# Kernel optimization log

Hardware: AMD Instinct MI355X
Metric: run time of the kernel (lower is better)

Reference implementation:

```python
import jax, jax.numpy as jnp
import numpy as np

B, S, M, D, H, L, FF = 2, 1024, 1024, 512, 8, 4, 2048
HD = D // H  # head dim 64
EPS = 1e-6   # fast_transformers linear-attention eps
LN_EPS = 1e-5


def setup_inputs() -> dict:
    key = jax.random.key(0)
    keys = iter(jax.random.split(key, 64))
    def w(shape, s=0.02):
        return jax.random.normal(next(keys), shape, dtype=jnp.float32) * s
    inp = {
        "memory": jax.random.normal(next(keys), (B, M, D), dtype=jnp.float32),
        "target": jax.random.normal(next(keys), (B, S, D), dtype=jnp.float32),
    }
    for p in ("sa", "ca"):
        for n in ("q", "k", "v", "o"):
            inp[f"{p}_W{n}"] = w((L, D, D))
            inp[f"{p}_b{n}"] = jnp.zeros((L, D), jnp.float32)
    inp["ff_W1"] = w((L, D, FF)); inp["ff_b1"] = jnp.zeros((L, FF), jnp.float32)
    inp["ff_W2"] = w((L, FF, D)); inp["ff_b2"] = jnp.zeros((L, D), jnp.float32)
    for n in ("ln1", "ln2", "ln3"):
        inp[f"{n}_g"] = jnp.ones((L, D), jnp.float32)
        inp[f"{n}_b"] = jnp.zeros((L, D), jnp.float32)
    inp["lnf_g"] = jnp.ones((D,), jnp.float32)
    inp["lnf_b"] = jnp.zeros((D,), jnp.float32)
    return inp


def _ln(x, g, b):
    m = x.mean(-1, keepdims=True)
    v = ((x - m) ** 2).mean(-1, keepdims=True)
    return (x - m) / jnp.sqrt(v + LN_EPS) * g + b


def _phi(x):  # elu feature map: elu(x) + 1
    return jax.nn.elu(x) + 1.0


def _heads(x, W, b):  # [b,s,D] -> [b,s,H,HD]
    y = x @ W + b
    return y.reshape(y.shape[0], y.shape[1], H, HD)


def _causal_linear_attn(q, k, v):
    # q,k already feature-mapped. cumulative KV state per step.
    kv = jnp.cumsum(jnp.einsum('bshd,bshm->bshdm', k, v), axis=1)  # [B,S,H,HD,HD]
    z = jnp.cumsum(k, axis=1)                                      # [B,S,H,HD]
    num = jnp.einsum('bshd,bshdm->bshm', q, kv)
    den = jnp.einsum('bshd,bshd->bsh', q, z) + EPS
    return num / den[..., None]


def _cross_linear_attn(q, k, v):
    kv = jnp.einsum('bmhd,bmhv->bhdv', k, v)  # [B,H,HD,HD]
    z = k.sum(axis=1)                          # [B,H,HD]
    num = jnp.einsum('bshd,bhdv->bshv', q, kv)
    den = jnp.einsum('bshd,bhd->bsh', q, z) + EPS
    return num / den[..., None]


def reference(memory, target,
              sa_Wq, sa_bq, sa_Wk, sa_bk, sa_Wv, sa_bv, sa_Wo, sa_bo,
              ca_Wq, ca_bq, ca_Wk, ca_bk, ca_Wv, ca_bv, ca_Wo, ca_bo,
              ff_W1, ff_b1, ff_W2, ff_b2,
              ln1_g, ln1_b, ln2_g, ln2_b, ln3_g, ln3_b, lnf_g, lnf_b):
    x = target
    for i in range(L):
        # causal linear self-attention
        q = _phi(_heads(x, sa_Wq[i], sa_bq[i]))
        k = _phi(_heads(x, sa_Wk[i], sa_bk[i]))
        v = _heads(x, sa_Wv[i], sa_bv[i])
        a = _causal_linear_attn(q, k, v).reshape(B, S, D) @ sa_Wo[i] + sa_bo[i]
        x = _ln(x + a, ln1_g[i], ln1_b[i])
        # linear cross-attention over memory
        q = _phi(_heads(x, ca_Wq[i], ca_bq[i]))
        k = _phi(_heads(memory, ca_Wk[i], ca_bk[i]))
        v = _heads(memory, ca_Wv[i], ca_bv[i])
        a = _cross_linear_attn(q, k, v).reshape(B, S, D) @ ca_Wo[i] + ca_bo[i]
        x = _ln(x + a, ln2_g[i], ln2_b[i])
        # gelu FFN
        y = jax.nn.gelu(x @ ff_W1[i] + ff_b1[i], approximate=False) @ ff_W2[i] + ff_b2[i]
        x = _ln(x + y, ln3_g[i], ln3_b[i])
    return _ln(x, lnf_g, lnf_b)
```

## Files before the change

### kernel.cpp

```cpp
#include <hip/hip_runtime.h>
#include <hip/hip_bf16.h>
#include <math.h>


typedef unsigned short u16;
typedef __bf16 bf16x8 __attribute__((ext_vector_type(8)));
typedef float f32x4v __attribute__((ext_vector_type(4)));

#define DEVI __device__ __forceinline__

DEVI float bf2f(u16 u) { return __uint_as_float(((unsigned)u) << 16); }
DEVI u16 f2bf(float f) {
  unsigned u = __float_as_uint(f);
  u += 0x7FFFu + ((u >> 16) & 1u);
  return (u16)(u >> 16);
}

__global__ __launch_bounds__(256) void transpose_f2b(
    const float* __restrict__ in, u16* __restrict__ out, int K, int N)
{
  __shared__ float tile[64 * 65];
  const size_t mat = (size_t)blockIdx.z * K * N;
  const int n0 = blockIdx.x * 64, k0 = blockIdx.y * 64;
  const int t = threadIdx.x;
#pragma unroll
  for (int p = 0; p < 16; ++p) {
    const int e = t + p * 256;
    const int lk = e >> 6, ln = e & 63;
    tile[lk * 65 + ln] = in[mat + (size_t)(k0 + lk) * N + n0 + ln];
  }
  __syncthreads();
#pragma unroll
  for (int p = 0; p < 16; ++p) {
    const int e = t + p * 256;
    const int ln = e >> 6, lk = e & 63;
    out[mat + (size_t)(n0 + ln) * K + k0 + lk] = f2bf(tile[lk * 65 + ln]);
  }
}

template<int ADT, int CDT>
__global__ __launch_bounds__(256) void gemm64(
    const void* __restrict__ A0, const void* __restrict__ A1, const void* __restrict__ A2,
    const u16* __restrict__ W0, const u16* __restrict__ W1, const u16* __restrict__ W2,
    const float* __restrict__ b0, const float* __restrict__ b1, const float* __restrict__ b2,
    void* __restrict__ C0, void* __restrict__ C1, void* __restrict__ C2,
    int acts, int N, int K, int lognyb)
{
  constexpr int LDT = 72;
  __shared__ __align__(16) u16 As[64 * LDT];
  __shared__ __align__(16) u16 Bs[64 * LDT];
  const int tid = threadIdx.x;
  const int by = blockIdx.y;
  const int seg = by >> lognyb;
  const int ny = by & ((1 << lognyb) - 1);
  const void* Av = seg == 0 ? A0 : (seg == 1 ? A1 : A2);
  const u16*  W  = seg == 0 ? W0 : (seg == 1 ? W1 : W2);
  const float* bias = seg == 0 ? b0 : (seg == 1 ? b1 : b2);
  void* Cv = seg == 0 ? C0 : (seg == 1 ? C1 : C2);
  const int act = (acts >> (2 * seg)) & 3;

  const int bm0 = blockIdx.x * 64, bn0 = ny * 64;
  const int lane = tid & 63, wid = tid >> 6;
  const int wr = wid >> 1, wc = wid & 1;
  const int l15 = lane & 15, lg = lane >> 4;
  const int srow = tid >> 2, scg = (tid & 3) * 16;
  f32x4v acc[2][2] = {};

  for (int k0 = 0; k0 < K; k0 += 64) {
    if (ADT == 0) {
      const float* A = (const float*)Av;
      const float* ap = &A[(size_t)(bm0 + srow) * K + k0 + scg];
#pragma unroll
      for (int i = 0; i < 4; ++i) {
        const float4 v = *(const float4*)&ap[i * 4];
        *(ushort4*)&As[srow * LDT + scg + i * 4] =
            make_ushort4(f2bf(v.x), f2bf(v.y), f2bf(v.z), f2bf(v.w));
      }
    } else {
      const u16* A = (const u16*)Av;
#pragma unroll
      for (int i = 0; i < 2; ++i)
        *(uint4*)&As[srow * LDT + scg + i * 8] =
            *(const uint4*)&A[(size_t)(bm0 + srow) * K + k0 + scg + i * 8];
    }
#pragma unroll
    for (int i = 0; i < 2; ++i)
      *(uint4*)&Bs[srow * LDT + scg + i * 8] =
          *(const uint4*)&W[(size_t)(bn0 + srow) * K + k0 + scg + i * 8];
    __syncthreads();
    bf16x8 af[2][2], bw[2][2];
#pragma unroll
    for (int kk = 0; kk < 2; ++kk) {
#pragma unroll
      for (int mm = 0; mm < 2; ++mm)
        af[kk][mm] = *(const bf16x8*)&As[(wr * 32 + mm * 16 + l15) * LDT + kk * 32 + lg * 8];
#pragma unroll
      for (int nn = 0; nn < 2; ++nn)
        bw[kk][nn] = *(const bf16x8*)&Bs[(wc * 32 + nn * 16 + l15) * LDT + kk * 32 + lg * 8];
    }
#pragma unroll
    for (int kk = 0; kk < 2; ++kk)
#pragma unroll
      for (int mm = 0; mm < 2; ++mm)
#pragma unroll
        for (int nn = 0; nn < 2; ++nn)
          acc[mm][nn] = __builtin_amdgcn_mfma_f32_16x16x32_bf16(af[kk][mm], bw[kk][nn], acc[mm][nn], 0, 0, 0);
    __syncthreads();
  }
#pragma unroll
  for (int nn = 0; nn < 2; ++nn) {
    const int col = bn0 + wc * 32 + nn * 16 + l15;
    const float bv = bias[col];
#pragma unroll
    for (int mm = 0; mm < 2; ++mm) {
#pragma unroll
      for (int r = 0; r < 4; ++r) {
        const int row = bm0 + wr * 32 + mm * 16 + lg * 4 + r;
        float v = acc[mm][nn][r] + bv;
        if (act == 1) v = v > 0.f ? v + 1.f : __expf(v);
        else if (act == 2) v = 0.5f * v * (1.f + erff(v * 0.70710678f));
        if (CDT == 0) ((float*)Cv)[(size_t)row * N + col] = v;
        else          ((u16*)Cv)[(size_t)row * N + col] = f2bf(v);
      }
    }
  }
}

__global__ __launch_bounds__(256) void lin_chunk_mfma(
    const float* __restrict__ kbuf, const float* __restrict__ vbuf,
    float* __restrict__ KVc, float* __restrict__ zc)
{
  constexpr int LDT = 72;
  __shared__ __align__(16) u16 Kt[64 * LDT];
  __shared__ __align__(16) u16 Vt[64 * LDT];
  const int c = blockIdx.x, bh = blockIdx.y;
  const int b = bh >> 3, h = bh & 7;
  const int t = threadIdx.x;
  const size_t rowbase = (size_t)(b * 1024 + c * 64);
  const int sp = t >> 4, colq = (t & 15) * 4;
#pragma unroll
  for (int pp = 0; pp < 2; ++pp) {
    const int s0 = pp * 32 + 2 * sp;
    const float4 ka = *(const float4*)&kbuf[(rowbase + s0) * 512 + h * 64 + colq];
    const float4 kb_ = *(const float4*)&kbuf[(rowbase + s0 + 1) * 512 + h * 64 + colq];
    const float4 va = *(const float4*)&vbuf[(rowbase + s0) * 512 + h * 64 + colq];
    const float4 vb_ = *(const float4*)&vbuf[(rowbase + s0 + 1) * 512 + h * 64 + colq];
    *(unsigned*)&Kt[(colq + 0) * LDT + s0] = (unsigned)f2bf(ka.x) | ((unsigned)f2bf(kb_.x) << 16);
    *(unsigned*)&Kt[(colq + 1) * LDT + s0] = (unsigned)f2bf(ka.y) | ((unsigned)f2bf(kb_.y) << 16);
    *(unsigned*)&Kt[(colq + 2) * LDT + s0] = (unsigned)f2bf(ka.z) | ((unsigned)f2bf(kb_.z) << 16);
    *(unsigned*)&Kt[(colq + 3) * LDT + s0] = (unsigned)f2bf(ka.w) | ((unsigned)f2bf(kb_.w) << 16);
    *(unsigned*)&Vt[(colq + 0) * LDT + s0] = (unsigned)f2bf(va.x) | ((unsigned)f2bf(vb_.x) << 16);
    *(unsigned*)&Vt[(colq + 1) * LDT + s0] = (unsigned)f2bf(va.y) | ((unsigned)f2bf(vb_.y) << 16);
    *(unsigned*)&Vt[(colq + 2) * LDT + s0] = (unsigned)f2bf(va.z) | ((unsigned)f2bf(vb_.z) << 16);
    *(unsigned*)&Vt[(colq + 3) * LDT + s0] = (unsigned)f2bf(va.w) | ((unsigned)f2bf(vb_.w) << 16);
  }
  __syncthreads();
  {
    const int zd = t >> 2, zg = t & 3;
    float zp = 0.f;
#pragma unroll
    for (int ss = 0; ss < 16; ++ss) zp += bf2f(Kt[zd * LDT + zg * 16 + ss]);
    zp += __shfl_xor(zp, 1, 64);
    zp += __shfl_xor(zp, 2, 64);
    if (zg == 0) zc[(size_t)(bh * 16 + c) * 64 + zd] = zp;
  }
  const int lane = t & 63, wid = t >> 6;
  const int wr = wid >> 1, wc = wid & 1;
  const int l15 = lane & 15, lg = lane >> 4;
  bf16x8 av[2][2], bk[2][2];
#pragma unroll
  for (int kk = 0; kk < 2; ++kk) {
#pragma unroll
    for (int mm = 0; mm < 2; ++mm)
      av[kk][mm] = *(const bf16x8*)&Vt[(wr * 32 + mm * 16 + l15) * LDT + kk * 32 + lg * 8];
#pragma unroll
    for (int nn = 0; nn < 2; ++nn)
      bk[kk][nn] = *(const bf16x8*)&Kt[(wc * 32 + nn * 16 + l15) * LDT + kk * 32 + lg * 8];
  }
  f32x4v acc[2][2] = {};
#pragma unroll
  for (int kk = 0; kk < 2; ++kk)
#pragma unroll
    for (int mm = 0; mm < 2; ++mm)
#pragma unroll
      for (int nn = 0; nn < 2; ++nn)
        acc[mm][nn] = __builtin_amdgcn_mfma_f32_16x16x32_bf16(av[kk][mm], bk[kk][nn], acc[mm][nn], 0, 0, 0);
  float* kvout = KVc + (size_t)(bh * 16 + c) * 4096;
#pragma unroll
  for (int mm = 0; mm < 2; ++mm)
#pragma unroll
    for (int r = 0; r < 4; ++r) {
      const int row = wr * 32 + mm * 16 + lg * 4 + r;
#pragma unroll
      for (int nn = 0; nn < 2; ++nn) {
        const int col = wc * 32 + nn * 16 + l15;
        kvout[row * 64 + col] = acc[mm][nn][r];
      }
    }
}

__global__ __launch_bounds__(256) void lin_scan_exclusive(
    float* __restrict__ KVc, float* __restrict__ zc,
    float* __restrict__ KVtot, float* __restrict__ ztot)
{
  const int grp = blockIdx.x, bh = blockIdx.y, t = threadIdx.x;
  const size_t base = (size_t)bh * 16 * 4096 + grp * 256 + t;
  float run = 0.f;
#pragma unroll
  for (int c = 0; c < 16; ++c) {
    const float tmp = KVc[base + (size_t)c * 4096];
    KVc[base + (size_t)c * 4096] = run;
    run += tmp;
  }
  KVtot[(size_t)bh * 4096 + grp * 256 + t] = run;
  if (grp == 0 && t < 64) {
    const size_t zb = (size_t)bh * 16 * 64 + t;
    float rz = 0.f;
#pragma unroll
    for (int c = 0; c < 16; ++c) {
      const float tmp = zc[zb + c * 64];
      zc[zb + c * 64] = rz;
      rz += tmp;
    }
    ztot[bh * 64 + t] = rz;
  }
}

__global__ __launch_bounds__(256) void sa_apply_mfma(
    const float* __restrict__ qbuf, const float* __restrict__ kbuf,
    const float* __restrict__ vbuf, const float* __restrict__ KVc,
    const float* __restrict__ zc, u16* __restrict__ out)
{
  constexpr int LDT = 72;
  __shared__ __align__(16) u16 Qs[64 * LDT];
  __shared__ __align__(16) u16 Ks[64 * LDT];
  __shared__ __align__(16) u16 Vt[64 * LDT];
  __shared__ __align__(16) u16 Ps[64 * LDT];
  __shared__ __align__(16) u16 KVs[64 * LDT];
  __shared__ float zp[64];
  __shared__ float den1[2][64];
  __shared__ float den2[64];
  const int c = blockIdx.x, bh = blockIdx.y;
  const int b = bh >> 3, h = bh & 7;
  const int t = threadIdx.x;
  const size_t rowbase = (size_t)(b * 1024 + c * 64);
  {
    const int srow = t >> 2, scg = (t & 3) * 16;
    const float* qp = &qbuf[(rowbase + srow) * 512 + h * 64 + scg];
    const float* kp = &kbuf[(rowbase + srow) * 512 + h * 64 + scg];
    const float* kvp = KVc + (size_t)(bh * 16 + c) * 4096 + srow * 64 + scg;
#pragma unroll
    for (int i = 0; i < 4; ++i) {
      const float4 a = *(const float4*)&qp[i * 4];
      *(ushort4*)&Qs[srow * LDT + scg + i * 4] = make_ushort4(f2bf(a.x), f2bf(a.y), f2bf(a.z), f2bf(a.w));
      const float4 bb = *(const float4*)&kp[i * 4];
      *(ushort4*)&Ks[srow * LDT + scg + i * 4] = make_ushort4(f2bf(bb.x), f2bf(bb.y), f2bf(bb.z), f2bf(bb.w));
      const float4 cc = *(const float4*)&kvp[i * 4];
      *(ushort4*)&KVs[srow * LDT + scg + i * 4] = make_ushort4(f2bf(cc.x), f2bf(cc.y), f2bf(cc.z), f2bf(cc.w));
    }
  }
  {
    const int sp = t >> 4, colq = (t & 15) * 4;
#pragma unroll
    for (int pp = 0; pp < 2; ++pp) {
      const int s0 = pp * 32 + 2 * sp;
      const float4 va = *(const float4*)&vbuf[(rowbase + s0) * 512 + h * 64 + colq];
      const float4 vb_ = *(const float4*)&vbuf[(rowbase + s0 + 1) * 512 + h * 64 + colq];
      *(unsigned*)&Vt[(colq + 0) * LDT + s0] = (unsigned)f2bf(va.x) | ((unsigned)f2bf(vb_.x) << 16);
      *(unsigned*)&Vt[(colq + 1) * LDT + s0] = (unsigned)f2bf(va.y) | ((unsigned)f2bf(vb_.y) << 16);
      *(unsigned*)&Vt[(colq + 2) * LDT + s0] = (unsigned)f2bf(va.z) | ((unsigned)f2bf(vb_.z) << 16);
      *(unsigned*)&Vt[(colq + 3) * LDT + s0] = (unsigned)f2bf(va.w) | ((unsigned)f2bf(vb_.w) << 16);
    }
  }
  if (t < 64) zp[t] = zc[(size_t)(bh * 16 + c) * 64 + t];
  __syncthreads();
  {
    const int di = t >> 2, dg = t & 3;
    float p2 = 0.f;
#pragma unroll
    for (int dd = 0; dd < 16; ++dd)
      p2 += bf2f(Qs[di * LDT + dg * 16 + dd]) * zp[dg * 16 + dd];
    p2 += __shfl_xor(p2, 1, 64);
    p2 += __shfl_xor(p2, 2, 64);
    if (dg == 0) den2[di] = p2;
  }
  const int lane = t & 63, wid = t >> 6;
  const int wr = wid >> 1, wc = wid & 1;
  const int l15 = lane & 15, lg = lane >> 4;
  bf16x8 af_q[2][2], bx[2][2];
#pragma unroll
  for (int kk = 0; kk < 2; ++kk) {
#pragma unroll
    for (int mm = 0; mm < 2; ++mm)
      af_q[kk][mm] = *(const bf16x8*)&Qs[(wr * 32 + mm * 16 + l15) * LDT + kk * 32 + lg * 8];
#pragma unroll
    for (int nn = 0; nn < 2; ++nn)
      bx[kk][nn] = *(const bf16x8*)&Ks[(wc * 32 + nn * 16 + l15) * LDT + kk * 32 + lg * 8];
  }
  f32x4v s_acc[2][2] = {};
#pragma unroll
  for (int kk = 0; kk < 2; ++kk)
#pragma unroll
    for (int mm = 0; mm < 2; ++mm)
#pragma unroll
      for (int nn = 0; nn < 2; ++nn)
        s_acc[mm][nn] = __builtin_amdgcn_mfma_f32_16x16x32_bf16(af_q[kk][mm], bx[kk][nn], s_acc[mm][nn], 0, 0, 0);
#pragma unroll
  for (int mm = 0; mm < 2; ++mm)
#pragma unroll
    for (int r = 0; r < 4; ++r) {
      const int row = wr * 32 + mm * 16 + lg * 4 + r;
      float dsum = 0.f;
#pragma unroll
      for (int nn = 0; nn < 2; ++nn) {
        const int col = wc * 32 + nn * 16 + l15;
        const float val = (col <= row) ? s_acc[mm][nn][r] : 0.f;
        Ps[row * LDT + col] = f2bf(val);
        dsum += val;
      }
      dsum += __shfl_xor(dsum, 1, 64);
      dsum += __shfl_xor(dsum, 2, 64);
      dsum += __shfl_xor(dsum, 4, 64);
      dsum += __shfl_xor(dsum, 8, 64);
      if (l15 == 0) den1[wc][row] = dsum;
    }
  __syncthreads();
  bf16x8 ap[2][2];
#pragma unroll
  for (int kk = 0; kk < 2; ++kk) {
#pragma unroll
    for (int mm = 0; mm < 2; ++mm)
      ap[kk][mm] = *(const bf16x8*)&Ps[(wr * 32 + mm * 16 + l15) * LDT + kk * 32 + lg * 8];
#pragma unroll
    for (int nn = 0; nn < 2; ++nn)
      bx[kk][nn] = *(const bf16x8*)&Vt[(wc * 32 + nn * 16 + l15) * LDT + kk * 32 + lg * 8];
  }
  f32x4v o_acc[2][2] = {};
#pragma unroll
  for (int kk = 0; kk < 2; ++kk)
#pragma unroll
    for (int mm = 0; mm < 2; ++mm)
#pragma unroll
      for (int nn = 0; nn < 2; ++nn)
        o_acc[mm][nn] = __builtin_amdgcn_mfma_f32_16x16x32_bf16(ap[kk][mm], bx[kk][nn], o_acc[mm][nn], 0, 0, 0);
#pragma unroll
  for (int kk = 0; kk < 2; ++kk)
#pragma unroll
    for (int nn = 0; nn < 2; ++nn)
      bx[kk][nn] = *(const bf16x8*)&KVs[(wc * 32 + nn * 16 + l15) * LDT + kk * 32 + lg * 8];
#pragma unroll
  for (int kk = 0; kk < 2; ++kk)
#pragma unroll
    for (int mm = 0; mm < 2; ++mm)
#pragma unroll
      for (int nn = 0; nn < 2; ++nn)
        o_acc[mm][nn] = __builtin_amdgcn_mfma_f32_16x16x32_bf16(af_q[kk][mm], bx[kk][nn], o_acc[mm][nn], 0, 0, 0);
#pragma unroll
  for (int mm = 0; mm < 2; ++mm)
#pragma unroll
    for (int r = 0; r < 4; ++r) {
      const int row = wr * 32 + mm * 16 + lg * 4 + r;
      const float rden = 1.f / (den1[0][row] + den1[1][row] + den2[row] + 1e-6f);
#pragma unroll
      for (int nn = 0; nn < 2; ++nn) {
        const int col = wc * 32 + nn * 16 + l15;
        out[(rowbase + row) * 512 + h * 64 + col] = f2bf(o_acc[mm][nn][r] * rden);
      }
    }
}

__global__ __launch_bounds__(256) void ca_apply_mfma(
    const float* __restrict__ qbuf, const float* __restrict__ KVtot,
    const float* __restrict__ ztot, u16* __restrict__ out)
{
  constexpr int LDT = 72;
  __shared__ __align__(16) u16 Qs[64 * LDT];
  __shared__ __align__(16) u16 KVs[64 * LDT];
  __shared__ float zt[64];
  __shared__ float den2[64];
  const int c = blockIdx.x, bh = blockIdx.y;
  const int b = bh >> 3, h = bh & 7;
  const int t = threadIdx.x;
  const size_t rowbase = (size_t)(b * 1024 + c * 64);
  {
    const int srow = t >> 2, scg = (t & 3) * 16;
    const float* qp = &qbuf[(rowbase + srow) * 512 + h * 64 + scg];
    const float* kvp = KVtot + (size_t)bh * 4096 + srow * 64 + scg;
#pragma unroll
    for (int i = 0; i < 4; ++i) {
      const float4 a = *(const float4*)&qp[i * 4];
      *(ushort4*)&Qs[srow * LDT + scg + i * 4] = make_ushort4(f2bf(a.x), f2bf(a.y), f2bf(a.z), f2bf(a.w));
      const float4 cc = *(const float4*)&kvp[i * 4];
      *(ushort4*)&KVs[srow * LDT + scg + i * 4] = make_ushort4(f2bf(cc.x), f2bf(cc.y), f2bf(cc.z), f2bf(cc.w));
    }
  }
  if (t < 64) zt[t] = ztot[bh * 64 + t];
  __syncthreads();
  {
    const int di = t >> 2, dg = t & 3;
    float p2 = 0.f;
#pragma unroll
    for (int dd = 0; dd < 16; ++dd)
      p2 += bf2f(Qs[di * LDT + dg * 16 + dd]) * zt[dg * 16 + dd];
    p2 += __shfl_xor(p2, 1, 64);
    p2 += __shfl_xor(p2, 2, 64);
    if (dg == 0) den2[di] = p2;
  }
  const int lane = t & 63, wid = t >> 6;
  const int wr = wid >> 1, wc = wid & 1;
  const int l15 = lane & 15, lg = lane >> 4;
  bf16x8 aq[2][2], bkv[2][2];
#pragma unroll
  for (int kk = 0; kk < 2; ++kk) {
#pragma unroll
    for (int mm = 0; mm < 2; ++mm)
      aq[kk][mm] = *(const bf16x8*)&Qs[(wr * 32 + mm * 16 + l15) * LDT + kk * 32 + lg * 8];
#pragma unroll
    for (int nn = 0; nn < 2; ++nn)
      bkv[kk][nn] = *(const bf16x8*)&KVs[(wc * 32 + nn * 16 + l15) * LDT + kk * 32 + lg * 8];
  }
  f32x4v o_acc[2][2] = {};
#pragma unroll
  for (int kk = 0; kk < 2; ++kk)
#pragma unroll
    for (int mm = 0; mm < 2; ++mm)
#pragma unroll
      for (int nn = 0; nn < 2; ++nn)
        o_acc[mm][nn] = __builtin_amdgcn_mfma_f32_16x16x32_bf16(aq[kk][mm], bkv[kk][nn], o_acc[mm][nn], 0, 0, 0);
  __syncthreads();
#pragma unroll
  for (int mm = 0; mm < 2; ++mm)
#pragma unroll
    for (int r = 0; r < 4; ++r) {
      const int row = wr * 32 + mm * 16 + lg * 4 + r;
      const float rden = 1.f / (den2[row] + 1e-6f);
#pragma unroll
      for (int nn = 0; nn < 2; ++nn) {
        const int col = wc * 32 + nn * 16 + l15;
        out[(rowbase + row) * 512 + h * 64 + col] = f2bf(o_acc[mm][nn][r] * rden);
      }
    }
}

__global__ __launch_bounds__(256) void ln_residual(
    float* __restrict__ x, const float* __restrict__ a,
    const float* __restrict__ g, const float* __restrict__ bt)
{
  const int t = threadIdx.x, lane = t & 63, w = t >> 6;
  const int row = blockIdx.x * 4 + w;
  float* xr = x + (size_t)row * 512;
  const float* ar = a + (size_t)row * 512;
  float4 x0 = *(const float4*)&xr[lane * 8];
  float4 x1 = *(const float4*)&xr[lane * 8 + 4];
  float4 a0 = *(const float4*)&ar[lane * 8];
  float4 a1 = *(const float4*)&ar[lane * 8 + 4];
  float v[8];
  v[0] = x0.x + a0.x; v[1] = x0.y + a0.y; v[2] = x0.z + a0.z; v[3] = x0.w + a0.w;
  v[4] = x1.x + a1.x; v[5] = x1.y + a1.y; v[6] = x1.z + a1.z; v[7] = x1.w + a1.w;
  float s = 0.f, sq = 0.f;
#pragma unroll
  for (int i = 0; i < 8; ++i) { s += v[i]; sq += v[i] * v[i]; }
#pragma unroll
  for (int off = 32; off > 0; off >>= 1) {
    s += __shfl_xor(s, off, 64);
    sq += __shfl_xor(sq, off, 64);
  }
  const float mean = s * (1.f / 512.f);
  const float var = sq * (1.f / 512.f) - mean * mean;
  const float rstd = rsqrtf(var + 1e-5f);
  float o[8];
#pragma unroll
  for (int i = 0; i < 8; ++i) {
    const int col = lane * 8 + i;
    o[i] = (v[i] - mean) * rstd * g[col] + bt[col];
  }
  *(float4*)&xr[lane * 8]     = make_float4(o[0], o[1], o[2], o[3]);
  *(float4*)&xr[lane * 8 + 4] = make_float4(o[4], o[5], o[6], o[7]);
}

__global__ __launch_bounds__(256) void ln_final(
    const float* __restrict__ x, const float* __restrict__ g,
    const float* __restrict__ bt, float* __restrict__ out)
{
  const int t = threadIdx.x, lane = t & 63, w = t >> 6;
  const int row = blockIdx.x * 4 + w;
  const float* xr = x + (size_t)row * 512;
  float4 x0 = *(const float4*)&xr[lane * 8];
  float4 x1 = *(const float4*)&xr[lane * 8 + 4];
  float v[8] = { x0.x, x0.y, x0.z, x0.w, x1.x, x1.y, x1.z, x1.w };
  float s = 0.f, sq = 0.f;
#pragma unroll
  for (int i = 0; i < 8; ++i) { s += v[i]; sq += v[i] * v[i]; }
#pragma unroll
  for (int off = 32; off > 0; off >>= 1) {
    s += __shfl_xor(s, off, 64);
    sq += __shfl_xor(sq, off, 64);
  }
  const float mean = s * (1.f / 512.f);
  const float var = sq * (1.f / 512.f) - mean * mean;
  const float rstd = rsqrtf(var + 1e-5f);
  float o[8];
#pragma unroll
  for (int i = 0; i < 8; ++i) {
    const int col = lane * 8 + i;
    o[i] = (v[i] - mean) * rstd * g[col] + bt[col];
  }
  *(float4*)&out[(size_t)row * 512 + lane * 8]     = make_float4(o[0], o[1], o[2], o[3]);
  *(float4*)&out[(size_t)row * 512 + lane * 8 + 4] = make_float4(o[4], o[5], o[6], o[7]);
}

extern "C" void kernel_launch(void* const* d_in, const int* in_sizes, int n_in,
                              void* d_out, int out_size, void* d_ws, size_t ws_size,
                              hipStream_t stream)
{
  (void)in_sizes; (void)n_in; (void)out_size; (void)ws_size;
  constexpr int Dm = 512, Lc = 4, FFc = 2048;

  const float* memory = (const float*)d_in[0];
  const float* target = (const float*)d_in[1];
  const float *saW[4], *sab[4], *caW[4], *cab[4];
  for (int j = 0; j < 4; ++j) {
    saW[j] = (const float*)d_in[2 + 2 * j];
    sab[j] = (const float*)d_in[3 + 2 * j];
    caW[j] = (const float*)d_in[10 + 2 * j];
    cab[j] = (const float*)d_in[11 + 2 * j];
  }
  const float* ffW1 = (const float*)d_in[18];
  const float* ffb1 = (const float*)d_in[19];
  const float* ffW2 = (const float*)d_in[20];
  const float* ffb2 = (const float*)d_in[21];
  const float* lng[4] = { (const float*)d_in[22], (const float*)d_in[24],
                          (const float*)d_in[26], (const float*)d_in[28] };
  const float* lnb[4] = { (const float*)d_in[23], (const float*)d_in[25],
                          (const float*)d_in[27], (const float*)d_in[29] };

  size_t off = 0;
  auto alloc = [&](size_t bytes) -> void* {
    void* p = (char*)d_ws + off;
    off += (bytes + 255) & ~(size_t)255;
    return p;
  };
  u16* WtS[4]; u16* WtC[4];
  for (int j = 0; j < 4; ++j) WtS[j] = (u16*)alloc((size_t)Lc * Dm * Dm * 2);
  for (int j = 0; j < 4; ++j) WtC[j] = (u16*)alloc((size_t)Lc * Dm * Dm * 2);
  u16* WtF1 = (u16*)alloc((size_t)Lc * Dm * FFc * 2);
  u16* WtF2 = (u16*)alloc((size_t)Lc * FFc * Dm * 2);
  float* x    = (float*)alloc((size_t)2048 * 512 * 4);
  float* qb   = (float*)alloc((size_t)2048 * 512 * 4);
  float* kb   = (float*)alloc((size_t)2048 * 512 * 4);
  float* vb   = (float*)alloc((size_t)2048 * 512 * 4);
  u16*   attn = (u16*)alloc((size_t)2048 * 512 * 2);
  u16*   ffh  = (u16*)alloc((size_t)2048 * 2048 * 2);
  float* KVc  = (float*)alloc((size_t)16 * 16 * 4096 * 4);
  float* zcb  = (float*)alloc((size_t)16 * 16 * 64 * 4);
  float* KVtot= (float*)alloc((size_t)16 * 4096 * 4);
  float* ztot = (float*)alloc((size_t)16 * 64 * 4);

  for (int j = 0; j < 4; ++j) {
    transpose_f2b<<<dim3(8, 8, 4), 256, 0, stream>>>(saW[j], WtS[j], Dm, Dm);
    transpose_f2b<<<dim3(8, 8, 4), 256, 0, stream>>>(caW[j], WtC[j], Dm, Dm);
  }
  transpose_f2b<<<dim3(32, 8, 4), 256, 0, stream>>>(ffW1, WtF1, Dm, FFc);
  transpose_f2b<<<dim3(8, 32, 4), 256, 0, stream>>>(ffW2, WtF2, FFc, Dm);

  hipMemcpyAsync(x, target, (size_t)2048 * 512 * 4, hipMemcpyDeviceToDevice, stream);

  for (int i = 0; i < Lc; ++i) {
    const size_t wo  = (size_t)i * Dm * Dm;
    const size_t wo1 = (size_t)i * Dm * FFc;
    const size_t wo2 = (size_t)i * FFc * Dm;
    gemm64<0, 0><<<dim3(32, 24), 256, 0, stream>>>(
        x, x, x, WtS[0] + wo, WtS[1] + wo, WtS[2] + wo,
        sab[0] + i * Dm, sab[1] + i * Dm, sab[2] + i * Dm,
        qb, kb, vb, 0x05, 512, 512, 3);
    lin_chunk_mfma<<<dim3(16, 16), 256, 0, stream>>>(kb, vb, KVc, zcb);
    lin_scan_exclusive<<<dim3(16, 16), 256, 0, stream>>>(KVc, zcb, KVtot, ztot);
    sa_apply_mfma<<<dim3(16, 16), 256, 0, stream>>>(qb, kb, vb, KVc, zcb, attn);
    gemm64<1, 0><<<dim3(32, 8), 256, 0, stream>>>(
        attn, attn, attn, WtS[3] + wo, WtS[3] + wo, WtS[3] + wo,
        sab[3] + i * Dm, sab[3] + i * Dm, sab[3] + i * Dm,
        qb, qb, qb, 0, 512, 512, 3);
    ln_residual<<<512, 256, 0, stream>>>(x, qb, lng[0] + i * Dm, lnb[0] + i * Dm);
    gemm64<0, 0><<<dim3(32, 24), 256, 0, stream>>>(
        x, memory, memory, WtC[0] + wo, WtC[1] + wo, WtC[2] + wo,
        cab[0] + i * Dm, cab[1] + i * Dm, cab[2] + i * Dm,
        qb, kb, vb, 0x05, 512, 512, 3);
    lin_chunk_mfma<<<dim3(16, 16), 256, 0, stream>>>(kb, vb, KVc, zcb);
    lin_scan_exclusive<<<dim3(16, 16), 256, 0, stream>>>(KVc, zcb, KVtot, ztot);
    ca_apply_mfma<<<dim3(16, 16), 256, 0, stream>>>(qb, KVtot, ztot, attn);
    gemm64<1, 0><<<dim3(32, 8), 256, 0, stream>>>(
        attn, attn, attn, WtC[3] + wo, WtC[3] + wo, WtC[3] + wo,
        cab[3] + i * Dm, cab[3] + i * Dm, cab[3] + i * Dm,
        qb, qb, qb, 0, 512, 512, 3);
    ln_residual<<<512, 256, 0, stream>>>(x, qb, lng[1] + i * Dm, lnb[1] + i * Dm);
    gemm64<0, 1><<<dim3(32, 32), 256, 0, stream>>>(
        x, x, x, WtF1 + wo1, WtF1 + wo1, WtF1 + wo1,
        ffb1 + i * FFc, ffb1 + i * FFc, ffb1 + i * FFc,
        ffh, ffh, ffh, 2, 2048, 512, 5);
    gemm64<1, 0><<<dim3(32, 8), 256, 0, stream>>>(
        ffh, ffh, ffh, WtF2 + wo2, WtF2 + wo2, WtF2 + wo2,
        ffb2 + i * Dm, ffb2 + i * Dm, ffb2 + i * Dm,
        qb, qb, qb, 0, 512, 2048, 3);
    ln_residual<<<512, 256, 0, stream>>>(x, qb, lng[2] + i * Dm, lnb[2] + i * Dm);
  }
  ln_final<<<512, 256, 0, stream>>>(x, lng[3], lnb[3], (float*)d_out);
}
```

Baseline: 682.1 us.

## Keep activations in bf16 between kernels and double-buffer GEMM shared tiles

LayerNorm now also writes a bf16 copy of the hidden state, memory and target are cast once up front, and Q/K/V projections are stored as bf16. GEMMs and attention kernels then read bf16 directly instead of loading fp32 and converting. The GEMM also gains a register-prefetched, double-buffered LDS pipeline with one barrier per K step and a launch-bounds occupancy hint. This halves intermediate traffic and removes conversion work, but rounds q/k/v before the attention kernels and uses more shared memory per block.

Result: faster. 605.6 us (-11.2%).

```diff
diff --git a/kernel.cpp b/kernel.cpp
--- a/kernel.cpp
+++ b/kernel.cpp
@@ -38,23 +38,37 @@
   }
 }
 
-template<int ADT, int CDT>
-__global__ __launch_bounds__(256) void gemm64(
-    const void* __restrict__ A0, const void* __restrict__ A1, const void* __restrict__ A2,
+__global__ __launch_bounds__(256) void cast_dual(
+    const float* __restrict__ in, float* __restrict__ fout, u16* __restrict__ bout)
+{
+  const int i = blockIdx.x * 256 + threadIdx.x;
+  const float4 a = ((const float4*)in)[i * 2];
+  const float4 b = ((const float4*)in)[i * 2 + 1];
+  if (fout) {
+    ((float4*)fout)[i * 2] = a;
+    ((float4*)fout)[i * 2 + 1] = b;
+  }
+  ((ushort4*)bout)[i * 2]     = make_ushort4(f2bf(a.x), f2bf(a.y), f2bf(a.z), f2bf(a.w));
+  ((ushort4*)bout)[i * 2 + 1] = make_ushort4(f2bf(b.x), f2bf(b.y), f2bf(b.z), f2bf(b.w));
+}
+
+template<int CDT>
+__global__ __launch_bounds__(256, 4) void gemm64(
+    const u16* __restrict__ A0, const u16* __restrict__ A1, const u16* __restrict__ A2,
     const u16* __restrict__ W0, const u16* __restrict__ W1, const u16* __restrict__ W2,
     const float* __restrict__ b0, const float* __restrict__ b1, const float* __restrict__ b2,
     void* __restrict__ C0, void* __restrict__ C1, void* __restrict__ C2,
     int acts, int N, int K, int lognyb)
 {
   constexpr int LDT = 72;
-  __shared__ __align__(16) u16 As[64 * LDT];
-  __shared__ __align__(16) u16 Bs[64 * LDT];
+  __shared__ __align__(16) u16 As[2][64 * LDT];
+  __shared__ __align__(16) u16 Bs[2][64 * LDT];
   const int tid = threadIdx.x;
   const int by = blockIdx.y;
   const int seg = by >> lognyb;
   const int ny = by & ((1 << lognyb) - 1);
-  const void* Av = seg == 0 ? A0 : (seg == 1 ? A1 : A2);
-  const u16*  W  = seg == 0 ? W0 : (seg == 1 ? W1 : W2);
+  const u16* A = seg == 0 ? A0 : (seg == 1 ? A1 : A2);
+  const u16* W = seg == 0 ? W0 : (seg == 1 ? W1 : W2);
   const float* bias = seg == 0 ? b0 : (seg == 1 ? b1 : b2);
   void* Cv = seg == 0 ? C0 : (seg == 1 ? C1 : C2);
   const int act = (acts >> (2 * seg)) & 3;
@@ -64,39 +78,38 @@
   const int wr = wid >> 1, wc = wid & 1;
   const int l15 = lane & 15, lg = lane >> 4;
   const int srow = tid >> 2, scg = (tid & 3) * 16;
+  const u16* Ap = A + (size_t)(bm0 + srow) * K + scg;
+  const u16* Wp = W + (size_t)(bn0 + srow) * K + scg;
+
+  uint4 ra0 = *(const uint4*)(Ap);
+  uint4 ra1 = *(const uint4*)(Ap + 8);
+  uint4 rb0 = *(const uint4*)(Wp);
+  uint4 rb1 = *(const uint4*)(Wp + 8);
+  *(uint4*)&As[0][srow * LDT + scg]     = ra0;
+  *(uint4*)&As[0][srow * LDT + scg + 8] = ra1;
+  *(uint4*)&Bs[0][srow * LDT + scg]     = rb0;
+  *(uint4*)&Bs[0][srow * LDT + scg + 8] = rb1;
+  __syncthreads();
+
   f32x4v acc[2][2] = {};
-
+  int cur = 0;
   for (int k0 = 0; k0 < K; k0 += 64) {
-    if (ADT == 0) {
-      const float* A = (const float*)Av;
-      const float* ap = &A[(size_t)(bm0 + srow) * K + k0 + scg];
-#pragma unroll
-      for (int i = 0; i < 4; ++i) {
-        const float4 v = *(const float4*)&ap[i * 4];
-        *(ushort4*)&As[srow * LDT + scg + i * 4] =
-            make_ushort4(f2bf(v.x), f2bf(v.y), f2bf(v.z), f2bf(v.w));
-      }
-    } else {
-      const u16* A = (const u16*)Av;
-#pragma unroll
-      for (int i = 0; i < 2; ++i)
-        *(uint4*)&As[srow * LDT + scg + i * 8] =
-            *(const uint4*)&A[(size_t)(bm0 + srow) * K + k0 + scg + i * 8];
-    }
-#pragma unroll
-    for (int i = 0; i < 2; ++i)
-      *(uint4*)&Bs[srow * LDT + scg + i * 8] =
-          *(const uint4*)&W[(size_t)(bn0 + srow) * K + k0 + scg + i * 8];
-    __syncthreads();
+    const bool more = (k0 + 64 < K);
+    if (more) {
+      ra0 = *(const uint4*)(Ap + k0 + 64);
+      ra1 = *(const uint4*)(Ap + k0 + 72);
+      rb0 = *(const uint4*)(Wp + k0 + 64);
+      rb1 = *(const uint4*)(Wp + k0 + 72);
+    }
     bf16x8 af[2][2], bw[2][2];
 #pragma unroll
     for (int kk = 0; kk < 2; ++kk) {
 #pragma unroll
       for (int mm = 0; mm < 2; ++mm)
-        af[kk][mm] = *(const bf16x8*)&As[(wr * 32 + mm * 16 + l15) * LDT + kk * 32 + lg * 8];
+        af[kk][mm] = *(const bf16x8*)&As[cur][(wr * 32 + mm * 16 + l15) * LDT + kk * 32 + lg * 8];
 #pragma unroll
       for (int nn = 0; nn < 2; ++nn)
-        bw[kk][nn] = *(const bf16x8*)&Bs[(wc * 32 + nn * 16 + l15) * LDT + kk * 32 + lg * 8];
+        bw[kk][nn] = *(const bf16x8*)&Bs[cur][(wc * 32 + nn * 16 + l15) * LDT + kk * 32 + lg * 8];
     }
 #pragma unroll
     for (int kk = 0; kk < 2; ++kk)
@@ -105,7 +118,14 @@
 #pragma unroll
         for (int nn = 0; nn < 2; ++nn)
           acc[mm][nn] = __builtin_amdgcn_mfma_f32_16x16x32_bf16(af[kk][mm], bw[kk][nn], acc[mm][nn], 0, 0, 0);
+    if (more) {
+      *(uint4*)&As[cur ^ 1][srow * LDT + scg]     = ra0;
+      *(uint4*)&As[cur ^ 1][srow * LDT + scg + 8] = ra1;
+      *(uint4*)&Bs[cur ^ 1][srow * LDT + scg]     = rb0;
+      *(uint4*)&Bs[cur ^ 1][srow * LDT + scg + 8] = rb1;
+    }
     __syncthreads();
+    cur ^= 1;
   }
 #pragma unroll
   for (int nn = 0; nn < 2; ++nn) {
@@ -127,7 +147,7 @@
 }
 
 __global__ __launch_bounds__(256) void lin_chunk_mfma(
-    const float* __restrict__ kbuf, const float* __restrict__ vbuf,
+    const u16* __restrict__ kbuf, const u16* __restrict__ vbuf,
     float* __restrict__ KVc, float* __restrict__ zc)
 {
   constexpr int LDT = 72;
@@ -141,18 +161,18 @@
 #pragma unroll
   for (int pp = 0; pp < 2; ++pp) {
     const int s0 = pp * 32 + 2 * sp;
-    const float4 ka = *(const float4*)&kbuf[(rowbase + s0) * 512 + h * 64 + colq];
-    const float4 kb_ = *(const float4*)&kbuf[(rowbase + s0 + 1) * 512 + h * 64 + colq];
-    const float4 va = *(const float4*)&vbuf[(rowbase + s0) * 512 + h * 64 + colq];
-    const float4 vb_ = *(const float4*)&vbuf[(rowbase + s0 + 1) * 512 + h * 64 + colq];
-    *(unsigned*)&Kt[(colq + 0) * LDT + s0] = (unsigned)f2bf(ka.x) | ((unsigned)f2bf(kb_.x) << 16);
-    *(unsigned*)&Kt[(colq + 1) * LDT + s0] = (unsigned)f2bf(ka.y) | ((unsigned)f2bf(kb_.y) << 16);
-    *(unsigned*)&Kt[(colq + 2) * LDT + s0] = (unsigned)f2bf(ka.z) | ((unsigned)f2bf(kb_.z) << 16);
-    *(unsigned*)&Kt[(colq + 3) * LDT + s0] = (unsigned)f2bf(ka.w) | ((unsigned)f2bf(kb_.w) << 16);
-    *(unsigned*)&Vt[(colq + 0) * LDT + s0] = (unsigned)f2bf(va.x) | ((unsigned)f2bf(vb_.x) << 16);
-    *(unsigned*)&Vt[(colq + 1) * LDT + s0] = (unsigned)f2bf(va.y) | ((unsigned)f2bf(vb_.y) << 16);
-    *(unsigned*)&Vt[(colq + 2) * LDT + s0] = (unsigned)f2bf(va.z) | ((unsigned)f2bf(vb_.z) << 16);
-    *(unsigned*)&Vt[(colq + 3) * LDT + s0] = (unsigned)f2bf(va.w) | ((unsigned)f2bf(vb_.w) << 16);
+    const ushort4 ka = *(const ushort4*)&kbuf[(rowbase + s0) * 512 + h * 64 + colq];
+    const ushort4 kb_ = *(const ushort4*)&kbuf[(rowbase + s0 + 1) * 512 + h * 64 + colq];
+    const ushort4 va = *(const ushort4*)&vbuf[(rowbase + s0) * 512 + h * 64 + colq];
+    const ushort4 vb_ = *(const ushort4*)&vbuf[(rowbase + s0 + 1) * 512 + h * 64 + colq];
+    *(unsigned*)&Kt[(colq + 0) * LDT + s0] = (unsigned)ka.x | ((unsigned)kb_.x << 16);
+    *(unsigned*)&Kt[(colq + 1) * LDT + s0] = (unsigned)ka.y | ((unsigned)kb_.y << 16);
+    *(unsigned*)&Kt[(colq + 2) * LDT + s0] = (unsigned)ka.z | ((unsigned)kb_.z << 16);
+    *(unsigned*)&Kt[(colq + 3) * LDT + s0] = (unsigned)ka.w | ((unsigned)kb_.w << 16);
+    *(unsigned*)&Vt[(colq + 0) * LDT + s0] = (unsigned)va.x | ((unsigned)vb_.x << 16);
+    *(unsigned*)&Vt[(colq + 1) * LDT + s0] = (unsigned)va.y | ((unsigned)vb_.y << 16);
+    *(unsigned*)&Vt[(colq + 2) * LDT + s0] = (unsigned)va.z | ((unsigned)vb_.z << 16);
+    *(unsigned*)&Vt[(colq + 3) * LDT + s0] = (unsigned)va.w | ((unsigned)vb_.w << 16);
   }
   __syncthreads();
   {
@@ -227,8 +247,8 @@
 }
 
 __global__ __launch_bounds__(256) void sa_apply_mfma(
-    const float* __restrict__ qbuf, const float* __restrict__ kbuf,
-    const float* __restrict__ vbuf, const float* __restrict__ KVc,
+    const u16* __restrict__ qbuf, const u16* __restrict__ kbuf,
+    const u16* __restrict__ vbuf, const float* __restrict__ KVc,
     const float* __restrict__ zc, u16* __restrict__ out)
 {
   constexpr int LDT = 72;
@@ -246,15 +266,13 @@
   const size_t rowbase = (size_t)(b * 1024 + c * 64);
   {
     const int srow = t >> 2, scg = (t & 3) * 16;
-    const float* qp = &qbuf[(rowbase + srow) * 512 + h * 64 + scg];
-    const float* kp = &kbuf[(rowbase + srow) * 512 + h * 64 + scg];
+    *(uint4*)&Qs[srow * LDT + scg]     = *(const uint4*)&qbuf[(rowbase + srow) * 512 + h * 64 + scg];
+    *(uint4*)&Qs[srow * LDT + scg + 8] = *(const uint4*)&qbuf[(rowbase + srow) * 512 + h * 64 + scg + 8];
+    *(uint4*)&Ks[srow * LDT + scg]     = *(const uint4*)&kbuf[(rowbase + srow) * 512 + h * 64 + scg];
+    *(uint4*)&Ks[srow * LDT + scg + 8] = *(const uint4*)&kbuf[(rowbase + srow) * 512 + h * 64 + scg + 8];
     const float* kvp = KVc + (size_t)(bh * 16 + c) * 4096 + srow * 64 + scg;
 #pragma unroll
     for (int i = 0; i < 4; ++i) {
-      const float4 a = *(const float4*)&qp[i * 4];
-      *(ushort4*)&Qs[srow * LDT + scg + i * 4] = make_ushort4(f2bf(a.x), f2bf(a.y), f2bf(a.z), f2bf(a.w));
-      const float4 bb = *(const float4*)&kp[i * 4];
-      *(ushort4*)&Ks[srow * LDT + scg + i * 4] = make_ushort4(f2bf(bb.x), f2bf(bb.y), f2bf(bb.z), f2bf(bb.w));
       const float4 cc = *(const float4*)&kvp[i * 4];
       *(ushort4*)&KVs[srow * LDT + scg + i * 4] = make_ushort4(f2bf(cc.x), f2bf(cc.y), f2bf(cc.z), f2bf(cc.w));
     }
@@ -264,12 +282,12 @@
 #pragma unroll
     for (int pp = 0; pp < 2; ++pp) {
       const int s0 = pp * 32 + 2 * sp;
-      const float4 va = *(const float4*)&vbuf[(rowbase + s0) * 512 + h * 64 + colq];
-      const float4 vb_ = *(const float4*)&vbuf[(rowbase + s0 + 1) * 512 + h * 64 + colq];
-      *(unsigned*)&Vt[(colq + 0) * LDT + s0] = (unsigned)f2bf(va.x) | ((unsigned)f2bf(vb_.x) << 16);
-      *(unsigned*)&Vt[(colq + 1) * LDT + s0] = (unsigned)f2bf(va.y) | ((unsigned)f2bf(vb_.y) << 16);
-      *(unsigned*)&Vt[(colq + 2) * LDT + s0] = (unsigned)f2bf(va.z) | ((unsigned)f2bf(vb_.z) << 16);
-      *(unsigned*)&Vt[(colq + 3) * LDT + s0] = (unsigned)f2bf(va.w) | ((unsigned)f2bf(vb_.w) << 16);
+      const ushort4 va = *(const ushort4*)&vbuf[(rowbase + s0) * 512 + h * 64 + colq];
+      const ushort4 vb_ = *(const ushort4*)&vbuf[(rowbase + s0 + 1) * 512 + h * 64 + colq];
+      *(unsigned*)&Vt[(colq + 0) * LDT + s0] = (unsigned)va.x | ((unsigned)vb_.x << 16);
+      *(unsigned*)&Vt[(colq + 1) * LDT + s0] = (unsigned)va.y | ((unsigned)vb_.y << 16);
+      *(unsigned*)&Vt[(colq + 2) * LDT + s0] = (unsigned)va.z | ((unsigned)vb_.z << 16);
+      *(unsigned*)&Vt[(colq + 3) * LDT + s0] = (unsigned)va.w | ((unsigned)vb_.w << 16);
     }
   }
   if (t < 64) zp[t] = zc[(size_t)(bh * 16 + c) * 64 + t];
@@ -370,7 +388,7 @@
 }
 
 __global__ __launch_bounds__(256) void ca_apply_mfma(
-    const float* __restrict__ qbuf, const float* __restrict__ KVtot,
+    const u16* __restrict__ qbuf, const float* __restrict__ KVtot,
     const float* __restrict__ ztot, u16* __restrict__ out)
 {
   constexpr int LDT = 72;
@@ -384,12 +402,11 @@
   const size_t rowbase = (size_t)(b * 1024 + c * 64);
   {
     const int srow = t >> 2, scg = (t & 3) * 16;
-    const float* qp = &qbuf[(rowbase + srow) * 512 + h * 64 + scg];
+    *(uint4*)&Qs[srow * LDT + scg]     = *(const uint4*)&qbuf[(rowbase + srow) * 512 + h * 64 + scg];
+    *(uint4*)&Qs[srow * LDT + scg + 8] = *(const uint4*)&qbuf[(rowbase + srow) * 512 + h * 64 + scg + 8];
     const float* kvp = KVtot + (size_t)bh * 4096 + srow * 64 + scg;
 #pragma unroll
     for (int i = 0; i < 4; ++i) {
-      const float4 a = *(const float4*)&qp[i * 4];
-      *(ushort4*)&Qs[srow * LDT + scg + i * 4] = make_ushort4(f2bf(a.x), f2bf(a.y), f2bf(a.z), f2bf(a.w));
       const float4 cc = *(const float4*)&kvp[i * 4];
       *(ushort4*)&KVs[srow * LDT + scg + i * 4] = make_ushort4(f2bf(cc.x), f2bf(cc.y), f2bf(cc.z), f2bf(cc.w));
     }
@@ -444,7 +461,8 @@
 
 __global__ __launch_bounds__(256) void ln_residual(
     float* __restrict__ x, const float* __restrict__ a,
-    const float* __restrict__ g, const float* __restrict__ bt)
+    const float* __restrict__ g, const float* __restrict__ bt,
+    u16* __restrict__ xb)
 {
   const int t = threadIdx.x, lane = t & 63, w = t >> 6;
   const int row = blockIdx.x * 4 + w;
@@ -476,6 +494,8 @@
   }
   *(float4*)&xr[lane * 8]     = make_float4(o[0], o[1], o[2], o[3]);
   *(float4*)&xr[lane * 8 + 4] = make_float4(o[4], o[5], o[6], o[7]);
+  *(ushort4*)&xb[(size_t)row * 512 + lane * 8]     = make_ushort4(f2bf(o[0]), f2bf(o[1]), f2bf(o[2]), f2bf(o[3]));
+  *(ushort4*)&xb[(size_t)row * 512 + lane * 8 + 4] = make_ushort4(f2bf(o[4]), f2bf(o[5]), f2bf(o[6]), f2bf(o[7]));
 }
 
 __global__ __launch_bounds__(256) void ln_final(
@@ -546,9 +566,12 @@
   u16* WtF1 = (u16*)alloc((size_t)Lc * Dm * FFc * 2);
   u16* WtF2 = (u16*)alloc((size_t)Lc * FFc * Dm * 2);
   float* x    = (float*)alloc((size_t)2048 * 512 * 4);
-  float* qb   = (float*)alloc((size_t)2048 * 512 * 4);
-  float* kb   = (float*)alloc((size_t)2048 * 512 * 4);
-  float* vb   = (float*)alloc((size_t)2048 * 512 * 4);
+  u16*   xb   = (u16*)alloc((size_t)2048 * 512 * 2);
+  u16*   memb = (u16*)alloc((size_t)2048 * 512 * 2);
+  u16*   qh   = (u16*)alloc((size_t)2048 * 512 * 2);
+  u16*   kh   = (u16*)alloc((size_t)2048 * 512 * 2);
+  u16*   vh   = (u16*)alloc((size_t)2048 * 512 * 2);
+  float* resid= (float*)alloc((size_t)2048 * 512 * 4);
   u16*   attn = (u16*)alloc((size_t)2048 * 512 * 2);
   u16*   ffh  = (u16*)alloc((size_t)2048 * 2048 * 2);
   float* KVc  = (float*)alloc((size_t)16 * 16 * 4096 * 4);
@@ -563,45 +586,46 @@
   transpose_f2b<<<dim3(32, 8, 4), 256, 0, stream>>>(ffW1, WtF1, Dm, FFc);
   transpose_f2b<<<dim3(8, 32, 4), 256, 0, stream>>>(ffW2, WtF2, FFc, Dm);
 
-  hipMemcpyAsync(x, target, (size_t)2048 * 512 * 4, hipMemcpyDeviceToDevice, stream);
+  cast_dual<<<512, 256, 0, stream>>>(target, x, xb);
+  cast_dual<<<512, 256, 0, stream>>>(memory, nullptr, memb);
 
   for (int i = 0; i < Lc; ++i) {
     const size_t wo  = (size_t)i * Dm * Dm;
     const size_t wo1 = (size_t)i * Dm * FFc;
     const size_t wo2 = (size_t)i * FFc * Dm;
-    gemm64<0, 0><<<dim3(32, 24), 256, 0, stream>>>(
-        x, x, x, WtS[0] + wo, WtS[1] + wo, WtS[2] + wo,
+    gemm64<1><<<dim3(32, 24), 256, 0, stream>>>(
+        xb, xb, xb, WtS[0] + wo, WtS[1] + wo, WtS[2] + wo,
         sab[0] + i * Dm, sab[1] + i * Dm, sab[2] + i * Dm,
-        qb, kb, vb, 0x05, 512, 512, 3);
-    lin_chunk_mfma<<<dim3(16, 16), 256, 0, stream>>>(kb, vb, KVc, zcb);
+        qh, kh, vh, 0x05, 512, 512, 3);
+    lin_chunk_mfma<<<dim3(16, 16), 256, 0, stream>>>(kh, vh, KVc, zcb);
     lin_scan_exclusive<<<dim3(16, 16), 256, 0, stream>>>(KVc, zcb, KVtot, ztot);
-    sa_apply_mfma<<<dim3(16, 16), 256, 0, stream>>>(qb, kb, vb, KVc, zcb, attn);
-    gemm64<1, 0><<<dim3(32, 8), 256, 0, stream>>>(
+    sa_apply_mfma<<<dim3(16, 16), 256, 0, stream>>>(qh, kh, vh, KVc, zcb, attn);
+    gemm64<0><<<dim3(32, 8), 256, 0, stream>>>(
         attn, attn, attn, WtS[3] + wo, WtS[3] + wo, WtS[3] + wo,
         sab[3] + i * Dm, sab[3] + i * Dm, sab[3] + i * Dm,
-        qb, qb, qb, 0, 512, 512, 3);
-    ln_residual<<<512, 256, 0, stream>>>(x, qb, lng[0] + i * Dm, lnb[0] + i * Dm);
-    gemm64<0, 0><<<dim3(32, 24), 256, 0, stream>>>(
-        x, memory, memory, WtC[0] + wo, WtC[1] + wo, WtC[2] + wo,
+        resid, resid, resid, 0, 512, 512, 3);
+    ln_residual<<<512, 256, 0, stream>>>(x, resid, lng[0] + i * Dm, lnb[0] + i * Dm, xb);
+    gemm64<1><<<dim3(32, 24), 256, 0, stream>>>(
+        xb, memb, memb, WtC[0] + wo, WtC[1] + wo, WtC[2] + wo,
         cab[0] + i * Dm, cab[1] + i * Dm, cab[2] + i * Dm,
-        qb, kb, vb, 0x05, 512, 512, 3);
-    lin_chunk_mfma<<<dim3(16, 16), 256, 0, stream>>>(kb, vb, KVc, zcb);
+        qh, kh, vh, 0x05, 512, 512, 3);
+    lin_chunk_mfma<<<dim3(16, 16), 256, 0, stream>>>(kh, vh, KVc, zcb);
     lin_scan_exclusive<<<dim3(16, 16), 256, 0, stream>>>(KVc, zcb, KVtot, ztot);
-    ca_apply_mfma<<<dim3(16, 16), 256, 0, stream>>>(qb, KVtot, ztot, attn);
-    gemm64<1, 0><<<dim3(32, 8), 256, 0, stream>>>(
+    ca_apply_mfma<<<dim3(16, 16), 256, 0, stream>>>(qh, KVtot, ztot, attn);
+    gemm64<0><<<dim3(32, 8), 256, 0, stream>>>(
         attn, attn, attn, WtC[3] + wo, WtC[3] + wo, WtC[3] + wo,
         cab[3] + i * Dm, cab[3] + i * Dm, cab[3] + i * Dm,
-        qb, qb, qb, 0, 512, 512, 3);
-    ln_residual<<<512, 256, 0, stream>>>(x, qb, lng[1] + i * Dm, lnb[1] + i * Dm);
-    gemm64<0, 1><<<dim3(32, 32), 256, 0, stream>>>(
-        x, x, x, WtF1 + wo1, WtF1 + wo1, WtF1 + wo1,
+        resid, resid, resid, 0, 512, 512, 3);
+    ln_residual<<<512, 256, 0, stream>>>(x, resid, lng[1] + i * Dm, lnb[1] + i * Dm, xb);
+    gemm64<1><<<dim3(32, 32), 256, 0, stream>>>(
+        xb, xb, xb, WtF1 + wo1, WtF1 + wo1, WtF1 + wo1,
         ffb1 + i * FFc, ffb1 + i * FFc, ffb1 + i * FFc,
         ffh, ffh, ffh, 2, 2048, 512, 5);
-    gemm64<1, 0><<<dim3(32, 8), 256, 0, stream>>>(
+    gemm64<0><<<dim3(32, 8), 256, 0, stream>>>(
         ffh, ffh, ffh, WtF2 + wo2, WtF2 + wo2, WtF2 + wo2,
         ffb2 + i * Dm, ffb2 + i * Dm, ffb2 + i * Dm,
-        qb, qb, qb, 0, 512, 2048, 3);
-    ln_residual<<<512, 256, 0, stream>>>(x, qb, lng[2] + i * Dm, lnb[2] + i * Dm);
+        resid, resid, resid, 0, 512, 2048, 3);
+    ln_residual<<<512, 256, 0, stream>>>(x, resid, lng[2] + i * Dm, lnb[2] + i * Dm, xb);
   }
   ln_final<<<512, 256, 0, stream>>>(x, lng[3], lnb[3], (float*)d_out);
 }
```
